# Optimization experiments

Measured on AMD Instinct MI355X. Metric: run time of the kernel, lower is better.

## Reference

```python
import jax, jax.numpy as jnp
import numpy as np

N = 50000        # nodes
E = 800000       # edges (before self loops)
F_IN = 78        # num_features_xd
H1 = 10          # heads of gcn1
OUT2 = 128       # output_dim of gcn2
G = 512          # graphs in batch
NEG_SLOPE = 0.2  # PyG GATConv default


def setup_inputs() -> dict:
    key = jax.random.key(0)
    ks = jax.random.split(key, 16)
    def glorot(k, shape, fan_in):
        return jax.random.normal(k, shape, jnp.float32) * (1.0 / np.sqrt(fan_in))
    inp = {}
    inp['x'] = jax.random.normal(ks[0], (N, F_IN), jnp.float32)
    inp['edge_index'] = jax.random.randint(ks[1], (2, E), 0, N, dtype=jnp.int32)
    inp['batch'] = jnp.sort(jax.random.randint(ks[2], (N,), 0, G, dtype=jnp.int32))
    inp['num_graphs'] = G
    # gcn1: GATConv(78 -> 78, heads=10, concat=True)
    inp['W1'] = glorot(ks[3], (F_IN, H1 * F_IN), F_IN)
    inp['a_src1'] = glorot(ks[4], (H1, F_IN), F_IN)
    inp['a_dst1'] = glorot(ks[5], (H1, F_IN), F_IN)
    inp['b1'] = jnp.zeros((H1 * F_IN,), jnp.float32)
    # gcn2: GATConv(780 -> 128, heads=1)
    inp['W2'] = glorot(ks[6], (H1 * F_IN, OUT2), H1 * F_IN)
    inp['a_src2'] = glorot(ks[7], (1, OUT2), OUT2)
    inp['a_dst2'] = glorot(ks[8], (1, OUT2), OUT2)
    inp['b2'] = jnp.zeros((OUT2,), jnp.float32)
    # fc_g1: Linear(128 -> 128)
    inp['fcW'] = glorot(ks[9], (OUT2, OUT2), OUT2)
    inp['fcb'] = jnp.zeros((OUT2,), jnp.float32)
    return inp


def _gat_layer(x, src, dst, W, a_src, a_dst, b, heads, out_dim):
    # x: [N, Fin] -> h: [N, heads, out_dim]
    n = x.shape[0]
    h = (x @ W).reshape(n, heads, out_dim)
    # per-node attention projections: [N, heads]
    alpha_src = jnp.einsum('nhf,hf->nh', h, a_src)
    alpha_dst = jnp.einsum('nhf,hf->nh', h, a_dst)
    # per-edge logits (message from src j to dst i): [Etot, heads]
    e = jax.nn.leaky_relu(alpha_src[src] + alpha_dst[dst], NEG_SLOPE)
    # segment softmax over edges grouped by destination node
    m = jax.ops.segment_max(e, dst, num_segments=n)
    m = jnp.where(jnp.isfinite(m), m, 0.0)
    ex = jnp.exp(e - m[dst])
    denom = jax.ops.segment_sum(ex, dst, num_segments=n)
    alpha = ex / (denom[dst] + 1e-16)
    # weighted message scatter: [N, heads, out_dim]
    out = jax.ops.segment_sum(h[src] * alpha[:, :, None], dst, num_segments=n)
    return out.reshape(n, heads * out_dim) + b


def reference(x, edge_index, batch, num_graphs, W1, a_src1, a_dst1, b1,
              W2, a_src2, a_dst2, b2, fcW, fcb):
    n = x.shape[0]
    # PyG GATConv add_self_loops=True
    loops = jnp.arange(n, dtype=edge_index.dtype)
    src = jnp.concatenate([edge_index[0], loops])
    dst = jnp.concatenate([edge_index[1], loops])
    # eval mode: dropouts are identity
    h = jax.nn.relu(_gat_layer(x, src, dst, W1, a_src1, a_dst1, b1, H1, F_IN))
    h = jax.nn.relu(_gat_layer(h, src, dst, W2, a_src2, a_dst2, b2, 1, OUT2))
    # global max pool over graphs
    pooled = jax.ops.segment_max(h, batch, num_segments=num_graphs)
    pooled = jnp.where(jnp.isfinite(pooled), pooled, 0.0)
    return jax.nn.relu(pooled @ fcW + fcb)
```

## Files before the change

### kernel.cpp

```cpp
#include <hip/hip_runtime.h>
#include <hip/hip_bf16.h>
#include <stdint.h>

typedef unsigned int uint32;
typedef unsigned short u16;
typedef __attribute__((ext_vector_type(8))) short bf16x8;
typedef __attribute__((ext_vector_type(4))) float f32x4;
typedef __attribute__((ext_vector_type(2))) float f32x2;
typedef uint32 u32x4 __attribute__((ext_vector_type(4)));

#define N_NODES 50000
#define NP      50048
#define N_EDGES 800000
#define ETOT    (N_EDGES + N_NODES)
#define F_INN   78
#define H1      10
#define D1      780
#define OUT2    128
#define NGRAPH  512
#define NEG_SLOPE 0.2f
#define PL40    ((size_t)NP * 40)

__device__ __forceinline__ float lrelu(float v) { return v > 0.f ? v : NEG_SLOPE * v; }
__device__ __forceinline__ u16 f2bfbits(float f) {
    return __bfloat16_as_ushort(__float2bfloat16(f));
}
__device__ __forceinline__ uint32 packbf(float lo, float hi) {
    return (uint32)f2bfbits(lo) | ((uint32)f2bfbits(hi) << 16);
}
__device__ __forceinline__ f32x2 bf2(uint32 u) {
    __hip_bfloat162 b = *reinterpret_cast<__hip_bfloat162*>(&u);
    float2 t = __bfloat1622float2(b);
    return (f32x2){t.x, t.y};
}
__device__ __forceinline__ int esrc(const int* ei, int e) { return e < N_EDGES ? ei[e] : e - N_EDGES; }
__device__ __forceinline__ int edst(const int* ei, int e) { return e < N_EDGES ? ei[N_EDGES + e] : e - N_EDGES; }

typedef __attribute__((address_space(1))) const uint32 guint;
typedef __attribute__((address_space(3))) uint32 luint;
__device__ __forceinline__ void cp16(uint32* lds, const uint32* g, int lane) {
    __builtin_amdgcn_global_load_lds((guint*)(g + lane * 4), (luint*)lds, 16, 0, 0);
}

#define NXP (N_NODES * 80)
__global__ __launch_bounds__(256) void prep_kernel(const float* __restrict__ x,
                                                   const float* __restrict__ W1,
                                                   const float* __restrict__ W2,
                                                   u16* __restrict__ xbp,
                                                   u16* __restrict__ w1p,
                                                   u16* __restrict__ w2p) {
    const int total = NXP + 10 * 80 * 80 + 10 * 128 * 80;
    for (int id = blockIdx.x * 256 + threadIdx.x; id < total; id += gridDim.x * 256) {
        if (id < NXP) {
            int n = id / 80, k = id - n * 80;
            xbp[id] = (k < 78) ? f2bfbits(x[n * 78 + k]) : ((k == 78) ? (u16)0x3F80 : (u16)0);
        } else if (id < NXP + 64000) {
            int t = id - NXP;
            int h = t / 6400, r = t - h * 6400;
            int n = r / 80, k = r - n * 80;
            w1p[t] = (n < 78 && k < 78) ? f2bfbits(W1[k * D1 + h * 78 + n]) : (u16)0;
        } else {
            int t = id - NXP - 64000;
            int h = t / 10240, r = t - h * 10240;
            int n = r / 80, k = r - n * 80;
            w2p[t] = (k < 78) ? f2bfbits(W2[(h * 78 + k) * OUT2 + n]) : (u16)0;
        }
    }
}

__global__ __launch_bounds__(256) void prep2_kernel(const float* __restrict__ W1,
                                                    const float* __restrict__ a_src1,
                                                    const float* __restrict__ a_dst1,
                                                    const float* __restrict__ W2,
                                                    const float* __restrict__ a_src2,
                                                    const float* __restrict__ a_dst2,
                                                    u16* __restrict__ VAT,
                                                    float* __restrict__ w2as,
                                                    float* __restrict__ w2ad) {
    int gid = blockIdx.x * 256 + threadIdx.x;
    int gs = gridDim.x * 256;
    for (int idx = gid; idx < 32 * 80; idx += gs) {
        int j = idx / 80, k = idx - j * 80;
        float s = 0.f;
        if (j < 20 && k < 78) {
            int h = (j < 10) ? j : j - 10;
            const float* vec = ((j < 10) ? a_src1 : a_dst1) + h * F_INN;
            const float* wrow = W1 + k * D1 + h * F_INN;
            for (int f = 0; f < F_INN; ++f) s = fmaf(wrow[f], vec[f], s);
            VAT[idx] = f2bfbits(s);
        } else {
            VAT[idx] = 0;
        }
    }
    for (int c = gid; c < D1; c += gs) {
        const float* r0 = W2 + (size_t)c * OUT2;
        float s = 0.f, d = 0.f;
        for (int j = 0; j < OUT2; ++j) {
            s = fmaf(r0[j], a_src2[j], s);
            d = fmaf(r0[j], a_dst2[j], d);
        }
        w2as[c] = s;
        w2ad[c] = d;
    }
}

__global__ __launch_bounds__(256) void alphas1x_kernel(const uint32* __restrict__ xbu,
                                                       const uint32* __restrict__ vatu,
                                                       float* __restrict__ asd1,
                                                       float* __restrict__ asrc) {
    __shared__ uint32 As[5136];
    __shared__ uint32 Bs[1296];
    int tid = threadIdx.x, lane = tid & 63, wv = tid >> 6;
    int row0 = blockIdx.x * 128;
    const uint32* aplane = xbu + (size_t)row0 * 40;

#pragma unroll
    for (int t = 0; t < 5; ++t)
        cp16(As + wv * 1280 + t * 256, aplane + wv * 1280 + t * 256, lane);
    if (wv == 0) {
#pragma unroll
        for (int t = 0; t < 5; ++t)
            cp16(Bs + t * 256, vatu + t * 256, lane);
    }
    __syncthreads();

    int l15 = lane & 15, quad = lane >> 4;
    const u16* Asu = (const u16*)As;
    const u16* Bsu = (const u16*)Bs;
    f32x4 acc[2][2];
#pragma unroll
    for (int mi = 0; mi < 2; ++mi)
#pragma unroll
        for (int nj = 0; nj < 2; ++nj) acc[mi][nj] = (f32x4){0.f, 0.f, 0.f, 0.f};

    int abase[2], bbase[2];
#pragma unroll
    for (int mi = 0; mi < 2; ++mi) abase[mi] = (wv * 32 + mi * 16 + l15) * 80 + quad * 8;
#pragma unroll
    for (int nj = 0; nj < 2; ++nj) bbase[nj] = (nj * 16 + l15) * 80 + quad * 8;

    bf16x8 z8 = {0, 0, 0, 0, 0, 0, 0, 0};
#pragma unroll
    for (int ks = 0; ks < 96; ks += 32) {
        bf16x8 a[2], b[2];
#pragma unroll
        for (int mi = 0; mi < 2; ++mi) {
            a[mi] = *(const bf16x8*)(Asu + abase[mi] + ks);
            if (ks == 64 && quad >= 2) a[mi] = z8;
        }
#pragma unroll
        for (int nj = 0; nj < 2; ++nj) b[nj] = *(const bf16x8*)(Bsu + bbase[nj] + ks);
#pragma unroll
        for (int mi = 0; mi < 2; ++mi)
#pragma unroll
            for (int nj = 0; nj < 2; ++nj)
                acc[mi][nj] = __builtin_amdgcn_mfma_f32_16x16x32_bf16(a[mi], b[nj], acc[mi][nj], 0, 0, 0);
    }

#pragma unroll
    for (int mi = 0; mi < 2; ++mi)
#pragma unroll
        for (int nj = 0; nj < 2; ++nj) {
            int col = nj * 16 + l15;
            if (col < 20) {
#pragma unroll
                for (int reg = 0; reg < 4; ++reg) {
                    int row = row0 + wv * 32 + mi * 16 + quad * 4 + reg;
                    if (row < N_NODES) {
                        asd1[(size_t)row * 20 + col] = acc[mi][nj][reg];
                        if (col < 10) asrc[(size_t)row * 12 + col] = acc[mi][nj][reg];
                    }
                }
            }
        }
}

__global__ void histrank_kernel(const int* __restrict__ ei, int* __restrict__ deg,
                                int* __restrict__ rank) {
    int e = blockIdx.x * 256 + threadIdx.x;
    if (e < ETOT) rank[e] = atomicAdd(&deg[edst(ei, e)], 1);
}

__global__ __launch_bounds__(256) void scan1_kernel(const int* __restrict__ deg,
                                                    int* __restrict__ row_ptr,
                                                    int* __restrict__ bsum) {
    __shared__ int buf[256];
    int tid = threadIdx.x;
    int i = blockIdx.x * 256 + tid;
    int v = (i < N_NODES) ? deg[i] : 0;
    buf[tid] = v;
    __syncthreads();
    for (int off = 1; off < 256; off <<= 1) {
        int t = (tid >= off) ? buf[tid - off] : 0;
        __syncthreads();
        buf[tid] += t;
        __syncthreads();
    }
    if (i < N_NODES) row_ptr[i] = buf[tid] - v;
    if (tid == 255) bsum[blockIdx.x] = buf[255];
}

__global__ __launch_bounds__(256) void scan2_kernel(const int* __restrict__ bsum,
                                                    int* __restrict__ boff) {
    __shared__ int buf[256];
    int tid = threadIdx.x;
    int v = (tid < 196) ? bsum[tid] : 0;
    buf[tid] = v;
    __syncthreads();
    for (int off = 1; off < 256; off <<= 1) {
        int t = (tid >= off) ? buf[tid - off] : 0;
        __syncthreads();
        buf[tid] += t;
        __syncthreads();
    }
    if (tid < 196) boff[tid] = buf[tid] - v;
}

__global__ __launch_bounds__(256) void scan3_kernel(int* __restrict__ row_ptr,
                                                    const int* __restrict__ boff) {
    int i = blockIdx.x * 256 + threadIdx.x;
    if (i < N_NODES) row_ptr[i] = row_ptr[i] + boff[blockIdx.x];
    if (i == 0) row_ptr[N_NODES] = ETOT;
}

__global__ void scatter_kernel(const int* __restrict__ ei, const int* __restrict__ row_ptr,
                               const int* __restrict__ rank, u16* __restrict__ src_arr) {
    int e = blockIdx.x * 256 + threadIdx.x;
    if (e < ETOT) {
        int d = edst(ei, e);
        src_arr[row_ptr[d] + rank[e]] = (u16)esrc(ei, e);
    }
}

struct G1 {
    float4 af;
    float2 af2;
    u32x4 xv[5];
    int valid;
};

__global__ __launch_bounds__(128) void agg1m_kernel(const int* __restrict__ row_ptr,
                                                    const u16* __restrict__ src_arr,
                                                    const float* __restrict__ asrc,
                                                    const float* __restrict__ asd1,
                                                    const uint32* __restrict__ xbu,
                                                    u16* __restrict__ aggb16) {
    __shared__ uint32 S[2][1536];
    int tid = threadIdx.x, lane = tid & 63, wv = tid >> 6;
    int ip = blockIdx.x * 2 + wv;
    int i0 = ip * 2, i1 = i0 + 1;
    int rs0 = row_ptr[i0], d0 = row_ptr[i0 + 1] - rs0;
    int rs1 = row_ptr[i1], d1 = row_ptr[i1 + 1] - rs1;
    uint32* xt32 = S[wv];
    uint32* wm32 = xt32 + 1280;
    int l15 = lane & 15, quad = lane >> 4;
    int slot = lane & 31, half = lane >> 5;
    u32x4 z4 = {0, 0, 0, 0};
    if (lane < 24) *(u32x4*)(wm32 + 160 + lane * 4) = z4;
    uint32 selv = (l15 & 1) ? 0x07060302u : 0x05040100u;
    int hp = l15 >> 1;
    int pa1 = (quad * 8 + 4 * hp) & 31;
    int pa2 = (pa1 + 4) & 31;

    float dstv0[10], dstv1[10];
#pragma unroll
    for (int q = 0; q < 10; ++q) dstv0[q] = asd1[(size_t)i0 * 20 + 10 + q];
#pragma unroll
    for (int q = 0; q < 10; ++q) dstv1[q] = asd1[(size_t)i1 * 20 + 10 + q];

    auto gatherrows = [&](int s, int cnt, G1& g) {
        g.valid = slot < cnt;
        int srow = g.valid ? s : 0;
        const float* arow = asrc + (size_t)srow * 12;
        if (half == 0) {
            if (g.valid) { g.af = *(const float4*)(arow); g.af2 = *(const float2*)(arow + 4); }
        } else {
            if (g.valid) {
                float2 t0 = *(const float2*)(arow + 6);
                float2 t1 = *(const float2*)(arow + 8);
                g.af = make_float4(t0.x, t0.y, t1.x, t1.y);
            }
        }
#pragma unroll
        for (int t = 0; t < 5; ++t) {
            int c4 = 2 * t + half;
            g.xv[t] = z4;
            if (g.valid) g.xv[t] = *(const u32x4*)(xbu + (size_t)srow * 40 + c4 * 4);
        }
    };

    auto stage = [&](const G1& g, const float* dstv) {
        if (half == 0) {
            uint32 u0 = 0, u1 = 0, u2 = 0;
            if (g.valid) {
                u0 = packbf(__expf(lrelu(g.af.x + dstv[0])), __expf(lrelu(g.af.y + dstv[1])));
                u1 = packbf(__expf(lrelu(g.af.z + dstv[2])), __expf(lrelu(g.af.w + dstv[3])));
                u2 = packbf(__expf(lrelu(g.af2.x + dstv[4])), __expf(lrelu(g.af2.y + dstv[5])));
            }
            wm32[0 * 32 + (slot & 31)] = u0;
            wm32[1 * 32 + ((slot + 4) & 31)] = u1;
            wm32[2 * 32 + ((slot + 8) & 31)] = u2;
        } else {
            uint32 u3 = 0, u4 = 0;
            if (g.valid) {
                u3 = packbf(__expf(lrelu(g.af.x + dstv[6])), __expf(lrelu(g.af.y + dstv[7])));
                u4 = packbf(__expf(lrelu(g.af.z + dstv[8])), __expf(lrelu(g.af.w + dstv[9])));
            }
            wm32[3 * 32 + ((slot + 12) & 31)] = u3;
            wm32[4 * 32 + ((slot + 16) & 31)] = u4;
        }
#pragma unroll
        for (int t = 0; t < 5; ++t) {
            int c4 = 2 * t + half;
            uint32* rowp = xt32 + (4 * c4) * 32;
#pragma unroll
            for (int k = 0; k < 4; ++k)
                rowp[k * 32 + ((slot + 16 * c4 + 4 * k) & 31)] = g.xv[t][k];
        }
    };

    auto domfma = [&](f32x4* acc) {
        int arow2 = hp * 32;
        u32x4 a0 = *(const u32x4*)(wm32 + arow2 + pa1);
        u32x4 a1 = *(const u32x4*)(wm32 + arow2 + pa2);
        u32x4 au = {__builtin_amdgcn_perm(a0[1], a0[0], selv),
                    __builtin_amdgcn_perm(a0[3], a0[2], selv),
                    __builtin_amdgcn_perm(a1[1], a1[0], selv),
                    __builtin_amdgcn_perm(a1[3], a1[2], selv)};
        bf16x8 af = *(bf16x8*)&au;
#pragma unroll
        for (int nt = 0; nt < 5; ++nt) {
            int browb = (nt * 8 + hp) * 32;
            u32x4 b0 = *(const u32x4*)(xt32 + browb + pa1);
            u32x4 b1 = *(const u32x4*)(xt32 + browb + pa2);
            u32x4 bu = {__builtin_amdgcn_perm(b0[1], b0[0], selv),
                        __builtin_amdgcn_perm(b0[3], b0[2], selv),
                        __builtin_amdgcn_perm(b1[1], b1[0], selv),
                        __builtin_amdgcn_perm(b1[3], b1[2], selv)};
            bf16x8 bf = *(bf16x8*)&bu;
            acc[nt] = __builtin_amdgcn_mfma_f32_16x16x32_bf16(af, bf, acc[nt], 0, 0, 0);
        }
    };

    auto writeout = [&](int i, f32x4* acc) {
        float rden[4];
#pragma unroll
        for (int reg = 0; reg < 4; ++reg) {
            float d = __shfl(acc[4][reg], (lane & 48) | 14, 64);
            rden[reg] = __builtin_amdgcn_rcpf(d);
        }
        size_t nb = (size_t)i * 80 + l15;
#pragma unroll
        for (int reg = 0; reg < 4; ++reg) {
            int head = quad * 4 + reg;
            if (head < 10) {
                u16* hpn = aggb16 + (size_t)head * (size_t)PL40 * 2 + nb;
#pragma unroll
                for (int nt = 0; nt < 5; ++nt) {
                    float v = acc[nt][reg] * rden[reg];
                    u16 b = f2bfbits(v);
                    if (nt == 4 && l15 >= 14) b = 0;
                    hpn[nt * 16] = b;
                }
            }
        }
    };

    f32x4 acc0[5], acc1[5];
#pragma unroll
    for (int nt = 0; nt < 5; ++nt) { acc0[nt] = (f32x4){0.f,0.f,0.f,0.f}; acc1[nt] = (f32x4){0.f,0.f,0.f,0.f}; }

    if (d0 <= 32 && d1 <= 32) {
        int s0 = (int)src_arr[rs0 + slot];
        int s1 = (int)src_arr[rs1 + slot];
        G1 g0, g1;
        gatherrows(s0, d0, g0);
        stage(g0, dstv0);
        gatherrows(s1, d1, g1);
        __builtin_amdgcn_wave_barrier();
        domfma(acc0);
        writeout(i0, acc0);
        __builtin_amdgcn_wave_barrier();
        stage(g1, dstv1);
        __builtin_amdgcn_wave_barrier();
        domfma(acc1);
        writeout(i1, acc1);
    } else {
        int rss[2] = {rs0, rs1}, dd[2] = {d0, d1}, ii[2] = {i0, i1};
#pragma unroll
        for (int n = 0; n < 2; ++n) {
            f32x4* acc = (n == 0) ? acc0 : acc1;
            const float* dv = (n == 0) ? dstv0 : dstv1;
            for (int base = 0; base < dd[n]; base += 32) {
                int cnt = min(dd[n] - base, 32);
                int s = (int)src_arr[rss[n] + base + slot];
                G1 g;
                gatherrows(s, cnt, g);
                stage(g, dv);
                __builtin_amdgcn_wave_barrier();
                domfma(acc);
                __builtin_amdgcn_wave_barrier();
            }
            writeout(ii[n], acc);
        }
    }
}

__global__ __launch_bounds__(256) void gemmf_kernel(const uint32* __restrict__ aggb,
                                                    const uint32* __restrict__ w1p,
                                                    const uint32* __restrict__ w2p,
                                                    const float* __restrict__ b1,
                                                    const float* __restrict__ w2as,
                                                    const float* __restrict__ w2ad,
                                                    u16* __restrict__ h2,
                                                    float* __restrict__ as2,
                                                    float* __restrict__ ad2) {
    __shared__ uint32 As[2568];
    __shared__ uint32 Bs1[3208];
    __shared__ uint32 Bs2[5128];
    __shared__ uint32 C1s[2568];
    int tid = threadIdx.x, lane = tid & 63, wv = tid >> 6;
    int row0 = blockIdx.x * 64;
    int l15 = lane & 15, quad = lane >> 4;
    const u16* Asu = (const u16*)As;
    const u16* B1u = (const u16*)Bs1;
    const u16* B2u = (const u16*)Bs2;
    const u16* C1u = (const u16*)C1s;
    u16* Cw = (u16*)C1s;

    f32x4 acc2[8];
#pragma unroll
    for (int nj = 0; nj < 8; ++nj) acc2[nj] = (f32x4){0.f, 0.f, 0.f, 0.f};
    float s2p[4] = {}, d2p[4] = {};

    int abase = (wv * 16 + l15) * 80 + quad * 8;
    int b1base[5];
#pragma unroll
    for (int nj = 0; nj < 5; ++nj) b1base[nj] = (nj * 16 + l15) * 80 + quad * 8;
    int b2base[8];
#pragma unroll
    for (int nj = 0; nj < 8; ++nj) b2base[nj] = (nj * 16 + l15) * 80 + quad * 8;
    bf16x8 z8 = {0, 0, 0, 0, 0, 0, 0, 0};
    int rl0 = wv * 16 + quad * 4;

    for (int h = 0; h < 10; ++h) {
        const uint32* aplane = aggb + (size_t)h * PL40 + (size_t)row0 * 40;
        const uint32* w1pl = w1p + (size_t)h * 3200;
        const uint32* w2pl = w2p + (size_t)h * 5120;
        for (int t = wv; t < 10; t += 4)
            cp16(As + t * 256, aplane + t * 256, lane);
        int tw0 = wv * 3, tw1 = (wv == 3) ? 12 : wv * 3 + 3;
        for (int t = tw0; t < tw1; ++t)
            cp16(Bs1 + t * 256, w1pl + t * 256, lane);
        if (wv == 3 && lane < 32)
            cp16(Bs1 + 12 * 256, w1pl + 12 * 256, lane);
#pragma unroll
        for (int t = 0; t < 5; ++t)
            cp16(Bs2 + (wv * 5 + t) * 256, w2pl + (wv * 5 + t) * 256, lane);
        __syncthreads();

        f32x4 acc1[5];
#pragma unroll
        for (int nj = 0; nj < 5; ++nj) acc1[nj] = (f32x4){0.f, 0.f, 0.f, 0.f};
#pragma unroll
        for (int ks = 0; ks < 96; ks += 32) {
            bf16x8 a = *(const bf16x8*)(Asu + abase + ks);
            if (ks == 64 && quad >= 2) a = z8;
#pragma unroll
            for (int nj = 0; nj < 5; ++nj) {
                bf16x8 b = *(const bf16x8*)(B1u + b1base[nj] + ks);
                acc1[nj] = __builtin_amdgcn_mfma_f32_16x16x32_bf16(a, b, acc1[nj], 0, 0, 0);
            }
        }
#pragma unroll
        for (int nj = 0; nj < 5; ++nj) {
            int col = nj * 16 + l15;
            if (col < 78) {
                int gc = h * 78 + col;
                float bia = b1[gc], was = w2as[gc], wad = w2ad[gc];
#pragma unroll
                for (int reg = 0; reg < 4; ++reg) {
                    float v = fmaxf(acc1[nj][reg] + bia, 0.f);
                    Cw[(rl0 + reg) * 80 + col] = f2bfbits(v);
                    s2p[reg] = fmaf(v, was, s2p[reg]);
                    d2p[reg] = fmaf(v, wad, d2p[reg]);
                }
            } else {
#pragma unroll
                for (int reg = 0; reg < 4; ++reg) Cw[(rl0 + reg) * 80 + col] = 0;
            }
        }
        __builtin_amdgcn_wave_barrier();
#pragma unroll
        for (int ks = 0; ks < 96; ks += 32) {
            bf16x8 a = *(const bf16x8*)(C1u + abase + ks);
            if (ks == 64 && quad >= 2) a = z8;
#pragma unroll
            for (int nj = 0; nj < 8; ++nj) {
                bf16x8 b = *(const bf16x8*)(B2u + b2base[nj] + ks);
                acc2[nj] = __builtin_amdgcn_mfma_f32_16x16x32_bf16(a, b, acc2[nj], 0, 0, 0);
            }
        }
        __syncthreads();
    }

#pragma unroll
    for (int nj = 0; nj < 8; ++nj) {
        int col = nj * 16 + l15;
#pragma unroll
        for (int reg = 0; reg < 4; ++reg) {
            int r = row0 + rl0 + reg;
            if (r < N_NODES) h2[(size_t)r * OUT2 + col] = f2bfbits(acc2[nj][reg]);
        }
    }
#pragma unroll
    for (int off = 1; off < 16; off <<= 1)
#pragma unroll
        for (int reg = 0; reg < 4; ++reg) {
            s2p[reg] += __shfl_xor(s2p[reg], off, 64);
            d2p[reg] += __shfl_xor(d2p[reg], off, 64);
        }
    if (l15 == 0) {
#pragma unroll
        for (int reg = 0; reg < 4; ++reg) {
            int r = row0 + rl0 + reg;
            if (r < N_NODES) {
                as2[r] = s2p[reg];
                ad2[r] = d2p[reg];
            }
        }
    }
}

__global__ __launch_bounds__(256) void agg2_kernel(const int* __restrict__ row_ptr,
                                                   const u16* __restrict__ src_arr,
                                                   const float* __restrict__ as2,
                                                   const float* __restrict__ ad2,
                                                   const uint32* __restrict__ h2u,
                                                   const float* __restrict__ b2,
                                                   const int* __restrict__ batch,
                                                   float* __restrict__ pooled) {
    __shared__ float w_sh[4][64];
    __shared__ int src_sh[4][64];
    __shared__ float red[4][128];
    __shared__ int gsh[4];
    int tid = threadIdx.x, lane = tid & 63, wv = tid >> 6;
    int i = blockIdx.x * 4 + wv;
    int rs = row_ptr[i], deg = row_ptr[i + 1] - rs;
    float ad2i = ad2[i];

    f32x2 acc = {0.f, 0.f};
    float den = 0.f;
    if (deg <= 64) {
        if (lane < deg) {
            int s = (int)src_arr[rs + lane];
            float w = __expf(lrelu(as2[s] + ad2i));
            den = w;
            w_sh[wv][lane] = w;
            src_sh[wv][lane] = s;
        }
        __builtin_amdgcn_wave_barrier();
#pragma unroll
        for (int off = 1; off < 64; off <<= 1) den += __shfl_xor(den, off, 64);
        float rden = __builtin_amdgcn_rcpf(den);
        int cnt = deg, eix = 0;
        for (; eix + 7 < cnt; eix += 8) {
            int ss[8];
            float ww[8];
            uint32 uu[8];
#pragma unroll
            for (int q = 0; q < 8; ++q) {
                ss[q] = src_sh[wv][eix + q];
                ww[q] = w_sh[wv][eix + q];
            }
#pragma unroll
            for (int q = 0; q < 8; ++q) uu[q] = h2u[(size_t)ss[q] * 64 + lane];
#pragma unroll
            for (int q = 0; q < 8; ++q) acc = ww[q] * bf2(uu[q]) + acc;
        }
        for (; eix < cnt; ++eix) {
            int s0 = src_sh[wv][eix];
            float w0 = w_sh[wv][eix];
            uint32 u0 = h2u[(size_t)s0 * 64 + lane];
            acc = w0 * bf2(u0) + acc;
        }
        acc *= rden;
    } else {
        for (int eix = lane; eix < deg; eix += 64)
            den += __expf(lrelu(as2[(int)src_arr[rs + eix]] + ad2i));
#pragma unroll
        for (int off = 1; off < 64; off <<= 1) den += __shfl_xor(den, off, 64);
        float rden = __builtin_amdgcn_rcpf(den);
        for (int base = 0; base < deg; base += 64) {
            int cnt = min(deg - base, 64);
            if (lane < cnt) {
                int s = (int)src_arr[rs + base + lane];
                w_sh[wv][lane] = __expf(lrelu(as2[s] + ad2i));
                src_sh[wv][lane] = s;
            }
            __builtin_amdgcn_wave_barrier();
            int eix = 0;
            for (; eix + 7 < cnt; eix += 8) {
                int ss[8];
                float ww[8];
                uint32 uu[8];
#pragma unroll
                for (int q = 0; q < 8; ++q) {
                    ss[q] = src_sh[wv][eix + q];
                    ww[q] = w_sh[wv][eix + q];
                }
#pragma unroll
                for (int q = 0; q < 8; ++q) uu[q] = h2u[(size_t)ss[q] * 64 + lane];
#pragma unroll
                for (int q = 0; q < 8; ++q) acc = ww[q] * bf2(uu[q]) + acc;
            }
            for (; eix < cnt; ++eix) {
                int s0 = src_sh[wv][eix];
                float w0 = w_sh[wv][eix];
                uint32 u0 = h2u[(size_t)s0 * 64 + lane];
                acc = w0 * bf2(u0) + acc;
            }
            __builtin_amdgcn_wave_barrier();
        }
        acc *= rden;
    }
    float2 bv = ((const float2*)b2)[lane];
    float v0 = fmaxf(acc.x + bv.x, 0.f);
    float v1 = fmaxf(acc.y + bv.y, 0.f);
    int g = batch[i];
    red[wv][2 * lane] = v0;
    red[wv][2 * lane + 1] = v1;
    if (lane == 0) gsh[wv] = g;
    __syncthreads();
    bool leader = true;
#pragma unroll
    for (int w2i = 0; w2i < 3; ++w2i)
        if (w2i < wv && gsh[w2i] == g) leader = false;
    if (leader) {
        float m0 = v0, m1 = v1;
#pragma unroll
        for (int w2i = 1; w2i < 4; ++w2i) {
            if (w2i > wv && gsh[w2i] == g) {
                m0 = fmaxf(m0, red[w2i][2 * lane]);
                m1 = fmaxf(m1, red[w2i][2 * lane + 1]);
            }
        }
        atomicMax((int*)&pooled[g * OUT2 + 2 * lane], __float_as_int(m0));
        atomicMax((int*)&pooled[g * OUT2 + 2 * lane + 1], __float_as_int(m1));
    }
}

__global__ __launch_bounds__(128) void fc_kernel(const float* __restrict__ pooled,
                                                 const float* __restrict__ fcW,
                                                 const float* __restrict__ fcb,
                                                 float* __restrict__ out) {
    int g = blockIdx.x, tid = threadIdx.x;
    __shared__ float p[128];
    p[tid] = pooled[g * OUT2 + tid];
    __syncthreads();
    float acc = fcb[tid];
    for (int k = 0; k < 128; ++k) acc = fmaf(p[k], fcW[k * OUT2 + tid], acc);
    out[g * OUT2 + tid] = fmaxf(acc, 0.f);
}

extern "C" void kernel_launch(void* const* d_in, const int* in_sizes, int n_in,
                              void* d_out, int out_size, void* d_ws, size_t ws_size,
                              hipStream_t stream) {
    const float* x      = (const float*)d_in[0];
    const int*   ei     = (const int*)d_in[1];
    const int*   batch  = (const int*)d_in[2];
    const float* W1     = (const float*)d_in[4];
    const float* a_src1 = (const float*)d_in[5];
    const float* a_dst1 = (const float*)d_in[6];
    const float* b1     = (const float*)d_in[7];
    const float* W2     = (const float*)d_in[8];
    const float* a_src2 = (const float*)d_in[9];
    const float* a_dst2 = (const float*)d_in[10];
    const float* b2     = (const float*)d_in[11];
    const float* fcW    = (const float*)d_in[12];
    const float* fcb    = (const float*)d_in[13];
    float* out = (float*)d_out;

    size_t off = 0;
    char* base = (char*)d_ws;
    auto alloc = [&](size_t bytes) -> void* {
        void* p = base + off;
        off += (bytes + 255) & ~(size_t)255;
        return p;
    };
    uint32* aggb  = (uint32*)alloc(PL40 * 10 * 4);
    u16* h2arena  = (u16*)alloc((size_t)N_NODES * OUT2 * 2);
    u16* h2   = h2arena;
    u16* xbp  = h2arena;
    float* asd1 = (float*)alloc((size_t)N_NODES * 20 * 4);
    float* asrc = (float*)alloc((size_t)N_NODES * 12 * 4);
    float* as2  = (float*)alloc((size_t)N_NODES * 4);
    float* ad2  = (float*)alloc((size_t)N_NODES * 4);
    u16* w1p    = (u16*)alloc((size_t)(10 * 80 * 80) * 2 + 1024);
    u16* w2p    = (u16*)alloc((size_t)(10 * 128 * 80) * 2);
    u16* VAT    = (u16*)alloc((size_t)32 * 80 * 2);
    float* w2as = (float*)alloc((size_t)D1 * 4);
    float* w2ad = (float*)alloc((size_t)D1 * 4);
    float* pooled = (float*)alloc((size_t)NGRAPH * OUT2 * 4);
    int* deg     = (int*)alloc((size_t)N_NODES * 4);
    int* row_ptr = (int*)alloc((size_t)(N_NODES + 1) * 4);
    int* rank    = (int*)alloc((size_t)ETOT * 4);
    u16* src_arr = (u16*)alloc((size_t)ETOT * 2);
    int* bsum    = (int*)alloc(196 * 4);
    int* boff    = (int*)alloc(196 * 4);

    hipMemsetAsync(deg, 0, (size_t)N_NODES * 4, stream);
    hipMemsetAsync(pooled, 0, (size_t)NGRAPH * OUT2 * 4, stream);

    prep_kernel<<<2048, 256, 0, stream>>>(x, W1, W2, xbp, w1p, w2p);
    prep2_kernel<<<8, 256, 0, stream>>>(W1, a_src1, a_dst1, W2, a_src2, a_dst2,
                                        VAT, w2as, w2ad);
    alphas1x_kernel<<<391, 256, 0, stream>>>((const uint32*)xbp, (const uint32*)VAT,
                                             asd1, asrc);
    histrank_kernel<<<(ETOT + 255) / 256, 256, 0, stream>>>(ei, deg, rank);
    scan1_kernel<<<196, 256, 0, stream>>>(deg, row_ptr, bsum);
    scan2_kernel<<<1, 256, 0, stream>>>(bsum, boff);
    scan3_kernel<<<196, 256, 0, stream>>>(row_ptr, boff);
    scatter_kernel<<<(ETOT + 255) / 256, 256, 0, stream>>>(ei, row_ptr, rank, src_arr);
    agg1m_kernel<<<N_NODES / 4, 128, 0, stream>>>(row_ptr, src_arr, asrc, asd1,
                                                  (const uint32*)xbp, (u16*)aggb);
    gemmf_kernel<<<NP / 64, 256, 0, stream>>>(aggb, (const uint32*)w1p, (const uint32*)w2p,
                                              b1, w2as, w2ad, h2, as2, ad2);
    agg2_kernel<<<N_NODES / 4, 256, 0, stream>>>(row_ptr, src_arr, as2, ad2,
                                                 (const uint32*)h2, b2, batch, pooled);
    fc_kernel<<<NGRAPH, 128, 0, stream>>>(pooled, fcW, fcb, out);
}
```

Measured before the change: 312.3 us.

## Load GEMM operands directly from global memory instead of staging in LDS

The fused two-layer GEMM kernel no longer copies the aggregated activations and both weight planes into shared memory each head iteration. MFMA operands are now read straight from global memory, which relies on L1/L2 caching of the shared weights. This drops most of the LDS footprint and the block-wide __syncthreads, which may raise occupancy. In exchange, every wave issues redundant uncached-in-LDS global loads for the weight tiles, and no explicit prefetch hides their latency.

```diff
diff --git a/kernel.cpp b/kernel.cpp
--- a/kernel.cpp
+++ b/kernel.cpp
@@ -415,16 +415,10 @@
                                                     u16* __restrict__ h2,
                                                     float* __restrict__ as2,
                                                     float* __restrict__ ad2) {
-    __shared__ uint32 As[2568];
-    __shared__ uint32 Bs1[3208];
-    __shared__ uint32 Bs2[5128];
     __shared__ uint32 C1s[2568];
     int tid = threadIdx.x, lane = tid & 63, wv = tid >> 6;
     int row0 = blockIdx.x * 64;
     int l15 = lane & 15, quad = lane >> 4;
-    const u16* Asu = (const u16*)As;
-    const u16* B1u = (const u16*)Bs1;
-    const u16* B2u = (const u16*)Bs2;
     const u16* C1u = (const u16*)C1s;
     u16* Cw = (u16*)C1s;
 
@@ -434,41 +428,29 @@
     float s2p[4] = {}, d2p[4] = {};
 
     int abase = (wv * 16 + l15) * 80 + quad * 8;
-    int b1base[5];
-#pragma unroll
-    for (int nj = 0; nj < 5; ++nj) b1base[nj] = (nj * 16 + l15) * 80 + quad * 8;
-    int b2base[8];
-#pragma unroll
-    for (int nj = 0; nj < 8; ++nj) b2base[nj] = (nj * 16 + l15) * 80 + quad * 8;
+    int bcol = l15 * 80 + quad * 8;
     bf16x8 z8 = {0, 0, 0, 0, 0, 0, 0, 0};
     int rl0 = wv * 16 + quad * 4;
 
+    const u16* Au  = (const u16*)aggb + (size_t)row0 * 80 + abase;
+    const u16* B1u = (const u16*)w1p + bcol;
+    const u16* B2u = (const u16*)w2p + bcol;
+
     for (int h = 0; h < 10; ++h) {
-        const uint32* aplane = aggb + (size_t)h * PL40 + (size_t)row0 * 40;
-        const uint32* w1pl = w1p + (size_t)h * 3200;
-        const uint32* w2pl = w2p + (size_t)h * 5120;
-        for (int t = wv; t < 10; t += 4)
-            cp16(As + t * 256, aplane + t * 256, lane);
-        int tw0 = wv * 3, tw1 = (wv == 3) ? 12 : wv * 3 + 3;
-        for (int t = tw0; t < tw1; ++t)
-            cp16(Bs1 + t * 256, w1pl + t * 256, lane);
-        if (wv == 3 && lane < 32)
-            cp16(Bs1 + 12 * 256, w1pl + 12 * 256, lane);
-#pragma unroll
-        for (int t = 0; t < 5; ++t)
-            cp16(Bs2 + (wv * 5 + t) * 256, w2pl + (wv * 5 + t) * 256, lane);
-        __syncthreads();
+        const u16* Ah  = Au  + (size_t)h * PL40 * 2;
+        const u16* B1h = B1u + h * 6400;
+        const u16* B2h = B2u + h * 10240;
 
         f32x4 acc1[5];
 #pragma unroll
         for (int nj = 0; nj < 5; ++nj) acc1[nj] = (f32x4){0.f, 0.f, 0.f, 0.f};
 #pragma unroll
         for (int ks = 0; ks < 96; ks += 32) {
-            bf16x8 a = *(const bf16x8*)(Asu + abase + ks);
+            bf16x8 a = *(const bf16x8*)(Ah + ks);
             if (ks == 64 && quad >= 2) a = z8;
 #pragma unroll
             for (int nj = 0; nj < 5; ++nj) {
-                bf16x8 b = *(const bf16x8*)(B1u + b1base[nj] + ks);
+                bf16x8 b = *(const bf16x8*)(B1h + nj * 1280 + ks);
                 acc1[nj] = __builtin_amdgcn_mfma_f32_16x16x32_bf16(a, b, acc1[nj], 0, 0, 0);
             }
         }
@@ -497,11 +479,11 @@
             if (ks == 64 && quad >= 2) a = z8;
 #pragma unroll
             for (int nj = 0; nj < 8; ++nj) {
-                bf16x8 b = *(const bf16x8*)(B2u + b2base[nj] + ks);
+                bf16x8 b = *(const bf16x8*)(B2h + nj * 1280 + ks);
                 acc2[nj] = __builtin_amdgcn_mfma_f32_16x16x32_bf16(a, b, acc2[nj], 0, 0, 0);
             }
         }
-        __syncthreads();
+        __builtin_amdgcn_wave_barrier();
     }
 
 #pragma unroll
```

After: 352.3 us. +12.8%, slower.

## Double gemmf row tile to 128 to reuse staged weights across two subtiles

Applied to the files above, without the earlier changes.

The fused two-layer GEMM kernel now handles 128 rows per block as two 64-row subtiles. Each head's W1 and W2 slices are staged into shared memory once and used for both subtiles, halving weight traffic per row. The staging code is split into helper lambdas and moved to the end of the loop, but barriers still serialize the loads with compute, so no real overlap is added. The grid is halved to 391 blocks while shared memory and accumulator registers grow, which may lower occupancy and leave some CUs underused.

```diff
diff --git a/kernel.cpp b/kernel.cpp
--- a/kernel.cpp
+++ b/kernel.cpp
@@ -415,12 +415,12 @@
                                                     u16* __restrict__ h2,
                                                     float* __restrict__ as2,
                                                     float* __restrict__ ad2) {
-    __shared__ uint32 As[2568];
+    __shared__ uint32 As[5128];
     __shared__ uint32 Bs1[3208];
     __shared__ uint32 Bs2[5128];
     __shared__ uint32 C1s[2568];
     int tid = threadIdx.x, lane = tid & 63, wv = tid >> 6;
-    int row0 = blockIdx.x * 64;
+    int row0 = blockIdx.x * 128;
     int l15 = lane & 15, quad = lane >> 4;
     const u16* Asu = (const u16*)As;
     const u16* B1u = (const u16*)Bs1;
@@ -428,12 +428,14 @@
     const u16* C1u = (const u16*)C1s;
     u16* Cw = (u16*)C1s;
 
-    f32x4 acc2[8];
-#pragma unroll
-    for (int nj = 0; nj < 8; ++nj) acc2[nj] = (f32x4){0.f, 0.f, 0.f, 0.f};
-    float s2p[4] = {}, d2p[4] = {};
-
-    int abase = (wv * 16 + l15) * 80 + quad * 8;
+    f32x4 acc2[2][8];
+#pragma unroll
+    for (int rt = 0; rt < 2; ++rt)
+#pragma unroll
+        for (int nj = 0; nj < 8; ++nj) acc2[rt][nj] = (f32x4){0.f, 0.f, 0.f, 0.f};
+    float s2p[2][4] = {}, d2p[2][4] = {};
+
+    int abase64 = (wv * 16 + l15) * 80 + quad * 8;
     int b1base[5];
 #pragma unroll
     for (int nj = 0; nj < 5; ++nj) b1base[nj] = (nj * 16 + l15) * 80 + quad * 8;
@@ -443,12 +445,14 @@
     bf16x8 z8 = {0, 0, 0, 0, 0, 0, 0, 0};
     int rl0 = wv * 16 + quad * 4;
 
-    for (int h = 0; h < 10; ++h) {
+    auto stageA = [&](int h) {
         const uint32* aplane = aggb + (size_t)h * PL40 + (size_t)row0 * 40;
+        for (int t = wv; t < 20; t += 4)
+            cp16(As + t * 256, aplane + t * 256, lane);
+    };
+    auto stageB = [&](int h) {
         const uint32* w1pl = w1p + (size_t)h * 3200;
         const uint32* w2pl = w2p + (size_t)h * 5120;
-        for (int t = wv; t < 10; t += 4)
-            cp16(As + t * 256, aplane + t * 256, lane);
         int tw0 = wv * 3, tw1 = (wv == 3) ? 12 : wv * 3 + 3;
         for (int t = tw0; t < tw1; ++t)
             cp16(Bs1 + t * 256, w1pl + t * 256, lane);
@@ -457,78 +461,94 @@
 #pragma unroll
         for (int t = 0; t < 5; ++t)
             cp16(Bs2 + (wv * 5 + t) * 256, w2pl + (wv * 5 + t) * 256, lane);
+    };
+
+    stageA(0);
+    stageB(0);
+    for (int h = 0; h < 10; ++h) {
         __syncthreads();
-
-        f32x4 acc1[5];
-#pragma unroll
-        for (int nj = 0; nj < 5; ++nj) acc1[nj] = (f32x4){0.f, 0.f, 0.f, 0.f};
-#pragma unroll
-        for (int ks = 0; ks < 96; ks += 32) {
-            bf16x8 a = *(const bf16x8*)(Asu + abase + ks);
-            if (ks == 64 && quad >= 2) a = z8;
+#pragma unroll
+        for (int rt = 0; rt < 2; ++rt) {
+            int abase = rt * 64 * 80 + abase64;
+            f32x4 acc1[5];
+#pragma unroll
+            for (int nj = 0; nj < 5; ++nj) acc1[nj] = (f32x4){0.f, 0.f, 0.f, 0.f};
+#pragma unroll
+            for (int ks = 0; ks < 96; ks += 32) {
+                bf16x8 a = *(const bf16x8*)(Asu + abase + ks);
+                if (ks == 64 && quad >= 2) a = z8;
+#pragma unroll
+                for (int nj = 0; nj < 5; ++nj) {
+                    bf16x8 b = *(const bf16x8*)(B1u + b1base[nj] + ks);
+                    acc1[nj] = __builtin_amdgcn_mfma_f32_16x16x32_bf16(a, b, acc1[nj], 0, 0, 0);
+                }
+            }
 #pragma unroll
             for (int nj = 0; nj < 5; ++nj) {
-                bf16x8 b = *(const bf16x8*)(B1u + b1base[nj] + ks);
-                acc1[nj] = __builtin_amdgcn_mfma_f32_16x16x32_bf16(a, b, acc1[nj], 0, 0, 0);
-            }
-        }
-#pragma unroll
-        for (int nj = 0; nj < 5; ++nj) {
+                int col = nj * 16 + l15;
+                if (col < 78) {
+                    int gc = h * 78 + col;
+                    float bia = b1[gc], was = w2as[gc], wad = w2ad[gc];
+#pragma unroll
+                    for (int reg = 0; reg < 4; ++reg) {
+                        float v = fmaxf(acc1[nj][reg] + bia, 0.f);
+                        Cw[(rl0 + reg) * 80 + col] = f2bfbits(v);
+                        s2p[rt][reg] = fmaf(v, was, s2p[rt][reg]);
+                        d2p[rt][reg] = fmaf(v, wad, d2p[rt][reg]);
+                    }
+                } else {
+#pragma unroll
+                    for (int reg = 0; reg < 4; ++reg) Cw[(rl0 + reg) * 80 + col] = 0;
+                }
+            }
+            __builtin_amdgcn_wave_barrier();
+#pragma unroll
+            for (int ks = 0; ks < 96; ks += 32) {
+                bf16x8 a = *(const bf16x8*)(C1u + abase64 + ks);
+                if (ks == 64 && quad >= 2) a = z8;
+#pragma unroll
+                for (int nj = 0; nj < 8; ++nj) {
+                    bf16x8 b = *(const bf16x8*)(B2u + b2base[nj] + ks);
+                    acc2[rt][nj] = __builtin_amdgcn_mfma_f32_16x16x32_bf16(a, b, acc2[rt][nj], 0, 0, 0);
+                }
+            }
+            __builtin_amdgcn_wave_barrier();
+        }
+        __syncthreads();
+        if (h < 9) { stageA(h + 1); stageB(h + 1); }
+    }
+
+#pragma unroll
+    for (int rt = 0; rt < 2; ++rt)
+#pragma unroll
+        for (int nj = 0; nj < 8; ++nj) {
             int col = nj * 16 + l15;
-            if (col < 78) {
-                int gc = h * 78 + col;
-                float bia = b1[gc], was = w2as[gc], wad = w2ad[gc];
-#pragma unroll
-                for (int reg = 0; reg < 4; ++reg) {
-                    float v = fmaxf(acc1[nj][reg] + bia, 0.f);
-                    Cw[(rl0 + reg) * 80 + col] = f2bfbits(v);
-                    s2p[reg] = fmaf(v, was, s2p[reg]);
-                    d2p[reg] = fmaf(v, wad, d2p[reg]);
+#pragma unroll
+            for (int reg = 0; reg < 4; ++reg) {
+                int r = row0 + rt * 64 + rl0 + reg;
+                if (r < N_NODES) h2[(size_t)r * OUT2 + col] = f2bfbits(acc2[rt][nj][reg]);
+            }
+        }
+#pragma unroll
+    for (int off = 1; off < 16; off <<= 1)
+#pragma unroll
+        for (int rt = 0; rt < 2; ++rt)
+#pragma unroll
+            for (int reg = 0; reg < 4; ++reg) {
+                s2p[rt][reg] += __shfl_xor(s2p[rt][reg], off, 64);
+                d2p[rt][reg] += __shfl_xor(d2p[rt][reg], off, 64);
+            }
+    if (l15 == 0) {
+#pragma unroll
+        for (int rt = 0; rt < 2; ++rt)
+#pragma unroll
+            for (int reg = 0; reg < 4; ++reg) {
+                int r = row0 + rt * 64 + rl0 + reg;
+                if (r < N_NODES) {
+                    as2[r] = s2p[rt][reg];
+                    ad2[r] = d2p[rt][reg];
                 }
-            } else {
-#pragma unroll
-                for (int reg = 0; reg < 4; ++reg) Cw[(rl0 + reg) * 80 + col] = 0;
-            }
-        }
-        __builtin_amdgcn_wave_barrier();
-#pragma unroll
-        for (int ks = 0; ks < 96; ks += 32) {
-            bf16x8 a = *(const bf16x8*)(C1u + abase + ks);
-            if (ks == 64 && quad >= 2) a = z8;
-#pragma unroll
-            for (int nj = 0; nj < 8; ++nj) {
-                bf16x8 b = *(const bf16x8*)(B2u + b2base[nj] + ks);
-                acc2[nj] = __builtin_amdgcn_mfma_f32_16x16x32_bf16(a, b, acc2[nj], 0, 0, 0);
-            }
-        }
-        __syncthreads();
-    }
-
-#pragma unroll
-    for (int nj = 0; nj < 8; ++nj) {
-        int col = nj * 16 + l15;
-#pragma unroll
-        for (int reg = 0; reg < 4; ++reg) {
-            int r = row0 + rl0 + reg;
-            if (r < N_NODES) h2[(size_t)r * OUT2 + col] = f2bfbits(acc2[nj][reg]);
-        }
-    }
-#pragma unroll
-    for (int off = 1; off < 16; off <<= 1)
-#pragma unroll
-        for (int reg = 0; reg < 4; ++reg) {
-            s2p[reg] += __shfl_xor(s2p[reg], off, 64);
-            d2p[reg] += __shfl_xor(d2p[reg], off, 64);
-        }
-    if (l15 == 0) {
-#pragma unroll
-        for (int reg = 0; reg < 4; ++reg) {
-            int r = row0 + rl0 + reg;
-            if (r < N_NODES) {
-                as2[r] = s2p[reg];
-                ad2[r] = d2p[reg];
-            }
-        }
+            }
     }
 }
 
@@ -724,8 +744,8 @@
     scatter_kernel<<<(ETOT + 255) / 256, 256, 0, stream>>>(ei, row_ptr, rank, src_arr);
     agg1m_kernel<<<N_NODES / 4, 128, 0, stream>>>(row_ptr, src_arr, asrc, asd1,
                                                   (const uint32*)xbp, (u16*)aggb);
-    gemmf_kernel<<<NP / 64, 256, 0, stream>>>(aggb, (const uint32*)w1p, (const uint32*)w2p,
-                                              b1, w2as, w2ad, h2, as2, ad2);
+    gemmf_kernel<<<NP / 128, 256, 0, stream>>>(aggb, (const uint32*)w1p, (const uint32*)w2p,
+                                               b1, w2as, w2ad, h2, as2, ad2);
     agg2_kernel<<<N_NODES / 4, 256, 0, stream>>>(row_ptr, src_arr, as2, ad2,
                                                  (const uint32*)h2, b2, batch, pooled);
     fc_kernel<<<NGRAPH, 128, 0, stream>>>(pooled, fcW, fcb, out);
```

Measured after the change: 306.4 us (median of 2 runs). Within noise of the previous version (-1.9%).
